# Kernel tuning notes

Measured on AMD Instinct MI355X. Metric: run time of the kernel, lower is better.

The kernel has to match this reference:

```python
import jax, jax.numpy as jnp
import numpy as np

NUM_MODULES, INP, OUT = 64, 256, 256
B, T = 2048, 64


def setup_inputs() -> dict:
    key = jax.random.key(0)
    k1, k2, k3, k4 = jax.random.split(key, 4)
    x = jax.random.normal(k1, (B, T, INP), dtype=jnp.float32)
    indices = jax.random.randint(k2, (B,), 0, NUM_MODULES)
    # torch.nn.Linear init: U(-1/sqrt(in), 1/sqrt(in)) for both weight and bias
    bound = 1.0 / np.sqrt(INP)
    W = jax.random.uniform(k3, (NUM_MODULES, OUT, INP), minval=-bound, maxval=bound, dtype=jnp.float32)
    b = jax.random.uniform(k4, (NUM_MODULES, OUT), minval=-bound, maxval=bound, dtype=jnp.float32)
    return {"x": x, "indices": indices, "W": W, "b": b}


def reference(x, indices, W, b):
    # Per-sample expert selection: gather each sample's weight/bias, batched matmul.
    Wg = W[indices]            # [B, OUT, INP]
    bg = b[indices]            # [B, OUT]
    y = jnp.einsum("bti,boi->bto", x, Wg) + bg[:, None, :]
    return y
```

## Files before the change

### kernel.cpp

```cpp
#include <hip/hip_runtime.h>
#include <hip/hip_bf16.h>

#define NMOD 64
#define INPD 256
#define OUTD 256
#define BATCH 2048
#define TT 64

typedef __attribute__((ext_vector_type(8))) short short8;
typedef __attribute__((ext_vector_type(4))) float floatx4;

__device__ __forceinline__ unsigned int pack2(float a, float b) {
    union { __hip_bfloat162 h; unsigned int u; } cv;
    cv.h = __float22bfloat162_rn(make_float2(a, b));
    return cv.u;
}

__global__ __launch_bounds__(256) void conv_w_kernel(const float* __restrict__ W,
                                                     uint4* __restrict__ Wp) {
    int gid  = blockIdx.x * 256 + threadIdx.x;
    int lane = gid & 63;
    int frag = (gid >> 6) & 15;
    int ks   = (gid >> 10) & 7;
    int e    = gid >> 13;

    int n = (frag >> 3) * 128 + (frag & 7) * 16 + (lane & 15);
    int k = ks * 32 + (lane >> 4) * 8;

    const float* p = W + ((size_t)e * OUTD + n) * INPD + k;
    float4 v0 = *reinterpret_cast<const float4*>(p);
    float4 v1 = *reinterpret_cast<const float4*>(p + 4);
    Wp[gid] = make_uint4(pack2(v0.x, v0.y), pack2(v0.z, v0.w),
                         pack2(v1.x, v1.y), pack2(v1.z, v1.w));
}

template <bool PRECONV>
__global__ __launch_bounds__(256) void moe_gemm_kernel(
    const float* __restrict__ x, const int* __restrict__ idx,
    const void* __restrict__ Wsrc, const float* __restrict__ bias,
    float* __restrict__ y) {

    __shared__ unsigned short lx[TT * INPD];

    const int b    = blockIdx.x;
    const int tid  = threadIdx.x;
    const int lane = tid & 63;
    const int w    = tid >> 6;
    const int e    = idx[b];
    const int l15  = lane & 15;
    const int kq   = lane >> 4;

    const float4* xin = reinterpret_cast<const float4*>(x + (size_t)b * TT * INPD);
    char* lxc = reinterpret_cast<char*>(lx);
#pragma unroll
    for (int r = 0; r < 16; ++r) {
        int fid  = r * 256 + tid;
        float4 v = xin[fid];
        int t    = fid >> 6;
        int k    = (fid & 63) * 4;
        int byte = t * 512 + ((k * 2) ^ ((t & 7) << 4));
        __builtin_assume((byte & 7) == 0);
        *reinterpret_cast<uint2*>(lxc + byte) = make_uint2(pack2(v.x, v.y), pack2(v.z, v.w));
    }
    __syncthreads();

    floatx4 acc[4][4] = {};

#pragma unroll
    for (int ks = 0; ks < 8; ++ks) {
        short8 af[4];
#pragma unroll
        for (int mi = 0; mi < 4; ++mi) {
            int t    = mi * 16 + l15;
            int byte = t * 512 + ((ks * 64 + kq * 16) ^ ((t & 7) << 4));
            __builtin_assume((byte & 15) == 0);
            af[mi] = *reinterpret_cast<const short8*>(lxc + byte);
        }
        short8 bf[4];
        if (PRECONV) {
            const unsigned short* wp = reinterpret_cast<const unsigned short*>(Wsrc)
                + (((size_t)e * 8 + ks) << 13) + (w << 11) + (lane << 3);
#pragma unroll
            for (int ni = 0; ni < 4; ++ni)
                bf[ni] = *reinterpret_cast<const short8*>(wp + (ni << 9));
        } else {
            const float* Wf = reinterpret_cast<const float*>(Wsrc) + (size_t)e * OUTD * INPD;
#pragma unroll
            for (int ni = 0; ni < 4; ++ni) {
                int n = w * 64 + ni * 16 + l15;
                int k = ks * 32 + kq * 8;
                const float* p = Wf + (size_t)n * INPD + k;
                float4 v0 = *reinterpret_cast<const float4*>(p);
                float4 v1 = *reinterpret_cast<const float4*>(p + 4);
                union { short8 s; uint4 u; } cv;
                cv.u = make_uint4(pack2(v0.x, v0.y), pack2(v0.z, v0.w),
                                  pack2(v1.x, v1.y), pack2(v1.z, v1.w));
                bf[ni] = cv.s;
            }
        }
#pragma unroll
        for (int mi = 0; mi < 4; ++mi)
#pragma unroll
            for (int ni = 0; ni < 4; ++ni)
                acc[mi][ni] = __builtin_amdgcn_mfma_f32_16x16x32_bf16(
                    bf[ni], af[mi], acc[mi][ni], 0, 0, 0);
    }

    const floatx4* bp = reinterpret_cast<const floatx4*>(bias + e * OUTD + w * 64) + kq;
    floatx4 bv[4];
#pragma unroll
    for (int ni = 0; ni < 4; ++ni)
        bv[ni] = bp[ni * 4];

    float* yb = y + ((size_t)b * TT + l15) * OUTD + w * 64 + kq * 4;
#pragma unroll
    for (int mi = 0; mi < 4; ++mi) {
        float* yrow = yb + mi * (16 * OUTD);
#pragma unroll
        for (int ni = 0; ni < 4; ++ni)
            *reinterpret_cast<floatx4*>(yrow + ni * 16) = acc[mi][ni] + bv[ni];
    }
}

extern "C" void kernel_launch(void* const* d_in, const int* in_sizes, int n_in,
                              void* d_out, int out_size, void* d_ws, size_t ws_size,
                              hipStream_t stream) {
    const float* x    = (const float*)d_in[0];
    const int*   idx  = (const int*)d_in[1];
    const float* W    = (const float*)d_in[2];
    const float* bias = (const float*)d_in[3];
    float*       y    = (float*)d_out;

    const size_t w_elems      = (size_t)NMOD * OUTD * INPD;
    const size_t w_bf16_bytes = w_elems * sizeof(unsigned short);

    if (ws_size >= w_bf16_bytes) {
        conv_w_kernel<<<(unsigned)(w_elems / 8 / 256), 256, 0, stream>>>(
            W, reinterpret_cast<uint4*>(d_ws));
        moe_gemm_kernel<true><<<BATCH, 256, 0, stream>>>(x, idx, d_ws, bias, y);
    } else {
        moe_gemm_kernel<false><<<BATCH, 256, 0, stream>>>(x, idx, (const void*)W, bias, y);
    }
}
```

Baseline: 88.84 us.

## Sort samples by expert so neighbouring blocks share weights; init accumulators with bias

Adds a single-block counting-sort kernel that orders batch samples by expert index, and the GEMM kernel maps blockIdx through that order. Blocks running together then mostly read the same expert's bf16 weights, which should improve L2 reuse. The bias is now loaded into the accumulators before the MFMA loop instead of being added in the epilogue, and launch bounds request 4 blocks per CU. The cost is one extra kernel launch and a dependent read of the order array.

```diff
diff --git a/kernel.cpp b/kernel.cpp
--- a/kernel.cpp
+++ b/kernel.cpp
@@ -34,21 +34,62 @@
                          pack2(v1.x, v1.y), pack2(v1.z, v1.w));
 }
 
+__global__ __launch_bounds__(1024) void sort_kernel(const int* __restrict__ idx,
+                                                    int* __restrict__ order) {
+    __shared__ int hist[NMOD];
+    const int tid = threadIdx.x;
+    if (tid < NMOD) hist[tid] = 0;
+    __syncthreads();
+
+    const int e0 = idx[tid];
+    const int e1 = idx[tid + 1024];
+    atomicAdd(&hist[e0], 1);
+    atomicAdd(&hist[e1], 1);
+    __syncthreads();
+
+    if (tid < 64) {
+        int v   = hist[tid];
+        int sum = v;
+#pragma unroll
+        for (int off = 1; off < 64; off <<= 1) {
+            int n = __shfl_up(sum, off, 64);
+            if (tid >= off) sum += n;
+        }
+        hist[tid] = sum - v;
+    }
+    __syncthreads();
+
+    int p0 = atomicAdd(&hist[e0], 1);
+    order[p0] = tid;
+    int p1 = atomicAdd(&hist[e1], 1);
+    order[p1] = tid + 1024;
+}
+
 template <bool PRECONV>
-__global__ __launch_bounds__(256) void moe_gemm_kernel(
+__global__ __launch_bounds__(256, 4) void moe_gemm_kernel(
     const float* __restrict__ x, const int* __restrict__ idx,
     const void* __restrict__ Wsrc, const float* __restrict__ bias,
-    float* __restrict__ y) {
+    float* __restrict__ y, const int* __restrict__ order) {
 
     __shared__ unsigned short lx[TT * INPD];
 
-    const int b    = blockIdx.x;
+    const int b    = PRECONV ? order[blockIdx.x] : blockIdx.x;
     const int tid  = threadIdx.x;
     const int lane = tid & 63;
     const int w    = tid >> 6;
     const int e    = idx[b];
     const int l15  = lane & 15;
     const int kq   = lane >> 4;
+
+    const floatx4* bp = reinterpret_cast<const floatx4*>(bias + e * OUTD + w * 64) + kq;
+    floatx4 acc[4][4];
+#pragma unroll
+    for (int ni = 0; ni < 4; ++ni) {
+        floatx4 bv = bp[ni * 4];
+#pragma unroll
+        for (int mi = 0; mi < 4; ++mi)
+            acc[mi][ni] = bv;
+    }
 
     const float4* xin = reinterpret_cast<const float4*>(x + (size_t)b * TT * INPD);
     char* lxc = reinterpret_cast<char*>(lx);
@@ -63,8 +104,6 @@
         *reinterpret_cast<uint2*>(lxc + byte) = make_uint2(pack2(v.x, v.y), pack2(v.z, v.w));
     }
     __syncthreads();
-
-    floatx4 acc[4][4] = {};
 
 #pragma unroll
     for (int ks = 0; ks < 8; ++ks) {
@@ -106,19 +145,13 @@
                     bf[ni], af[mi], acc[mi][ni], 0, 0, 0);
     }
 
-    const floatx4* bp = reinterpret_cast<const floatx4*>(bias + e * OUTD + w * 64) + kq;
-    floatx4 bv[4];
-#pragma unroll
-    for (int ni = 0; ni < 4; ++ni)
-        bv[ni] = bp[ni * 4];
-
     float* yb = y + ((size_t)b * TT + l15) * OUTD + w * 64 + kq * 4;
 #pragma unroll
     for (int mi = 0; mi < 4; ++mi) {
         float* yrow = yb + mi * (16 * OUTD);
 #pragma unroll
         for (int ni = 0; ni < 4; ++ni)
-            *reinterpret_cast<floatx4*>(yrow + ni * 16) = acc[mi][ni] + bv[ni];
+            *reinterpret_cast<floatx4*>(yrow + ni * 16) = acc[mi][ni];
     }
 }
 
@@ -133,12 +166,15 @@
 
     const size_t w_elems      = (size_t)NMOD * OUTD * INPD;
     const size_t w_bf16_bytes = w_elems * sizeof(unsigned short);
+    const size_t order_bytes  = (size_t)BATCH * sizeof(int);
 
-    if (ws_size >= w_bf16_bytes) {
+    if (ws_size >= w_bf16_bytes + order_bytes) {
+        int* order = reinterpret_cast<int*>((char*)d_ws + w_bf16_bytes);
         conv_w_kernel<<<(unsigned)(w_elems / 8 / 256), 256, 0, stream>>>(
             W, reinterpret_cast<uint4*>(d_ws));
-        moe_gemm_kernel<true><<<BATCH, 256, 0, stream>>>(x, idx, d_ws, bias, y);
+        sort_kernel<<<1, 1024, 0, stream>>>(idx, order);
+        moe_gemm_kernel<true><<<BATCH, 256, 0, stream>>>(x, idx, d_ws, bias, y, order);
     } else {
-        moe_gemm_kernel<false><<<BATCH, 256, 0, stream>>>(x, idx, (const void*)W, bias, y);
+        moe_gemm_kernel<false><<<BATCH, 256, 0, stream>>>(x, idx, (const void*)W, bias, y, nullptr);
     }
 }
```

Measured after the change: 77.60 us. 12.7% less time.
